# Optimization experiments

Hardware: AMD Instinct MI355X
Metric: run time of the kernel (lower is better)

## Reference

```python
import jax, jax.numpy as jnp
import numpy as np

NUM_HEADS = 16
D_MODEL = 1024


def setup_inputs() -> dict:
    key = jax.random.key(0)
    ks = jax.random.split(key, 12)
    B, S, D = 2, 2048, D_MODEL
    inp = {
        "query": jax.random.normal(ks[0], (B, S, D), dtype=jnp.float32),
        "key": jax.random.normal(ks[1], (B, S, D), dtype=jnp.float32),
        "value": jax.random.normal(ks[2], (B, S, D), dtype=jnp.float32),
        "mask": jax.random.randint(ks[3], (B, 1, S), 0, 2).astype(jnp.bool_),
    }
    # Linear layer params, stored as (in, out) so y = x @ W + b
    sd = 1.0 / np.sqrt(D)
    for i, nm in enumerate(["q", "k", "v", "o"]):
        inp[f"W{nm}"] = jax.random.uniform(ks[4 + 2 * i], (D, D), jnp.float32, -sd, sd)
        inp[f"b{nm}"] = jax.random.uniform(ks[5 + 2 * i], (D,), jnp.float32, -sd, sd)
    return inp


def _split_heads(x):
    # [B, S, D] -> [B, H, S, d_k]
    B, S, D = x.shape
    return x.reshape(B, S, NUM_HEADS, D // NUM_HEADS).transpose(0, 2, 1, 3)


def reference(query, key, value, mask, Wq, bq, Wk, bk, Wv, bv, Wo, bo):
    B, Sq, D = query.shape
    d_k = D // NUM_HEADS
    scale = 1.0 / np.sqrt(d_k)

    q = _split_heads(query @ Wq + bq)   # [B,H,Sq,dk]
    k = _split_heads(key @ Wk + bk)     # [B,H,Sk,dk]
    v = _split_heads(value @ Wv + bv)   # [B,H,Sk,dk]

    scores = jnp.einsum("bhqd,bhkd->bhqk", q, k) * scale  # [B,H,Sq,Sk]
    # mask: [B,1,Sk] bool, True = masked; broadcast over heads and queries
    scores = jnp.where(mask[:, None, :, :], -jnp.inf, scores)
    attn = jax.nn.softmax(scores, axis=-1)
    attn = jnp.nan_to_num(attn, nan=0.0)  # fully-masked rows -> 0 (matches torch)

    ctx = jnp.einsum("bhqk,bhkd->bhqd", attn, v)  # [B,H,Sq,dk]
    ctx = ctx.transpose(0, 2, 1, 3).reshape(B, Sq, D)  # combine heads
    out = ctx @ Wo + bo
    return out
```

## Files before the change

### kernel.cpp

```cpp
#include <hip/hip_runtime.h>


typedef unsigned short u16;
typedef __attribute__((ext_vector_type(8))) short bf16x8;
typedef __attribute__((ext_vector_type(4))) float f32x4;

static __device__ __forceinline__ u16 f2bf(float x) {
  union { float f; unsigned int i; } v; v.f = x;
  return (u16)((v.i + 0x8000u) >> 16);
}
static __device__ __forceinline__ float bf2f(u16 u) {
  union { unsigned int i; float f; } v; v.i = ((unsigned int)u) << 16; return v.f;
}

#define MFMA_B16(a, b, c) __builtin_amdgcn_mfma_f32_16x16x32_bf16((a), (b), (c), 0, 0, 0)

__global__ __launch_bounds__(256) void prep_w(
    const float* __restrict__ w0, const float* __restrict__ w1,
    const float* __restrict__ w2, const float* __restrict__ w3,
    u16* __restrict__ t0, u16* __restrict__ t1,
    u16* __restrict__ t2, u16* __restrict__ t3) {
  __shared__ u16 tile[64 * 68];
  const float* W; u16* T;
  switch (blockIdx.z) {
    case 0: W = w0; T = t0; break;
    case 1: W = w1; T = t1; break;
    case 2: W = w2; T = t2; break;
    default: W = w3; T = t3; break;
  }
  const int t = threadIdx.x;
  const int k0 = blockIdx.x * 64, n0 = blockIdx.y * 64;
#pragma unroll
  for (int it = 0; it < 4; ++it) {
    int idx = it * 256 + t;
    int r = idx >> 4, c4 = idx & 15;
    float4 v = *(const float4*)&W[(size_t)(k0 + r) * 1024 + n0 + c4 * 4];
    tile[r * 68 + c4 * 4 + 0] = f2bf(v.x);
    tile[r * 68 + c4 * 4 + 1] = f2bf(v.y);
    tile[r * 68 + c4 * 4 + 2] = f2bf(v.z);
    tile[r * 68 + c4 * 4 + 3] = f2bf(v.w);
  }
  __syncthreads();
#pragma unroll
  for (int it = 0; it < 2; ++it) {
    int idx = it * 256 + t;
    int n = idx >> 3, kc = idx & 7;
    bf16x8 pk;
#pragma unroll
    for (int j = 0; j < 8; ++j) pk[j] = (short)tile[(kc * 8 + j) * 68 + n];
    *(bf16x8*)&T[(size_t)(n0 + n) * 1024 + k0 + kc * 8] = pk;
  }
}

template <int MT, int AMODE, int OMODE>
__global__ __launch_bounds__(256) void gemm_bias(
    const void* a0v, const void* a1v, const void* a2v,
    const u16* __restrict__ Wt,
    const float* b0, const float* b1, const float* b2,
    void* o0, void* o1, void* o2) {
  __shared__ __align__(16) u16 As[MT * 32 * 32];
  __shared__ __align__(16) u16 Bs[128 * 32];
  const int t = threadIdx.x, wave = t >> 6, lane = t & 63;
  const int l15 = lane & 15, quad = lane >> 4;
  const int m0 = blockIdx.x * (MT * 32);
  const int n0 = blockIdx.y * 128;
  const int rg = (OMODE == 3) ? (n0 >> 10) : 0;
  const void* Av = (rg == 0) ? a0v : (rg == 1 ? a1v : a2v);
  const float* bp = (rg == 0) ? b0 : (rg == 1 ? b1 : b2);
  const int nb = (OMODE == 3) ? (n0 & 1023) : n0;
  const int wr = (wave >> 1) * (MT * 16), wc = (wave & 1) * 64;

  const f32x4 fz = {0.f, 0.f, 0.f, 0.f};
  f32x4 acc[MT][4];
#pragma unroll
  for (int mt = 0; mt < MT; ++mt)
#pragma unroll
    for (int nt = 0; nt < 4; ++nt) acc[mt][nt] = fz;

  float4 pa[MT / 2][2]; bf16x8 pab[MT / 2]; bf16x8 pb[2];
#pragma unroll
  for (int s = 0; s < MT / 2; ++s) {
    int idx = s * 256 + t, row = idx >> 2, seg = idx & 3;
    if (AMODE == 1) {
      const float* ap = (const float*)Av + (size_t)(m0 + row) * 1024 + seg * 8;
      pa[s][0] = *(const float4*)ap; pa[s][1] = *(const float4*)(ap + 4);
    } else {
      pab[s] = *(const bf16x8*)((const u16*)Av + (size_t)(m0 + row) * 1024 + seg * 8);
    }
  }
#pragma unroll
  for (int s = 0; s < 2; ++s) {
    int idx = s * 256 + t, row = idx >> 2, seg = idx & 3;
    pb[s] = *(const bf16x8*)&Wt[(size_t)(n0 + row) * 1024 + seg * 8];
  }

  for (int kb = 0; kb < 1024; kb += 32) {
    __syncthreads();
#pragma unroll
    for (int s = 0; s < MT / 2; ++s) {
      int idx = s * 256 + t, row = idx >> 2, seg = idx & 3;
      bf16x8 pk;
      if (AMODE == 1) {
        pk[0] = (short)f2bf(pa[s][0].x); pk[1] = (short)f2bf(pa[s][0].y);
        pk[2] = (short)f2bf(pa[s][0].z); pk[3] = (short)f2bf(pa[s][0].w);
        pk[4] = (short)f2bf(pa[s][1].x); pk[5] = (short)f2bf(pa[s][1].y);
        pk[6] = (short)f2bf(pa[s][1].z); pk[7] = (short)f2bf(pa[s][1].w);
      } else pk = pab[s];
      *(bf16x8*)&As[row * 32 + seg * 8] = pk;
    }
#pragma unroll
    for (int s = 0; s < 2; ++s) {
      int idx = s * 256 + t, row = idx >> 2, seg = idx & 3;
      *(bf16x8*)&Bs[row * 32 + seg * 8] = pb[s];
    }
    __syncthreads();
    const int kn = (kb + 32) & 1023;
#pragma unroll
    for (int s = 0; s < MT / 2; ++s) {
      int idx = s * 256 + t, row = idx >> 2, seg = idx & 3;
      if (AMODE == 1) {
        const float* ap = (const float*)Av + (size_t)(m0 + row) * 1024 + kn + seg * 8;
        pa[s][0] = *(const float4*)ap; pa[s][1] = *(const float4*)(ap + 4);
      } else {
        pab[s] = *(const bf16x8*)((const u16*)Av + (size_t)(m0 + row) * 1024 + kn + seg * 8);
      }
    }
#pragma unroll
    for (int s = 0; s < 2; ++s) {
      int idx = s * 256 + t, row = idx >> 2, seg = idx & 3;
      pb[s] = *(const bf16x8*)&Wt[(size_t)(n0 + row) * 1024 + kn + seg * 8];
    }
    bf16x8 a[MT], bfr[4];
#pragma unroll
    for (int mt = 0; mt < MT; ++mt)
      a[mt] = *(const bf16x8*)&As[(wr + mt * 16 + l15) * 32 + quad * 8];
#pragma unroll
    for (int nt = 0; nt < 4; ++nt)
      bfr[nt] = *(const bf16x8*)&Bs[(wc + nt * 16 + l15) * 32 + quad * 8];
#pragma unroll
    for (int mt = 0; mt < MT; ++mt)
#pragma unroll
      for (int nt = 0; nt < 4; ++nt)
        acc[mt][nt] = MFMA_B16(a[mt], bfr[nt], acc[mt][nt]);
  }

#pragma unroll
  for (int nt = 0; nt < 4; ++nt) {
    const int n = nb + wc + nt * 16 + l15;
    const float bv = bp[n];
#pragma unroll
    for (int mt = 0; mt < MT; ++mt)
#pragma unroll
      for (int r = 0; r < 4; ++r) {
        const int m = m0 + wr + mt * 16 + quad * 4 + r;
        const float val = acc[mt][nt][r] + bv;
        if (OMODE == 2) {
          ((float*)o0)[(size_t)m * 1024 + n] = val;
        } else if (OMODE == 0) {
          ((u16*)o0)[(size_t)m * 1024 + n] = f2bf(val);
        } else {
          if (rg == 0)      ((u16*)o0)[(size_t)m * 1024 + n] = f2bf(val);
          else if (rg == 1) ((u16*)o1)[(size_t)m * 1024 + n] = f2bf(val);
          else {
            const int h = n >> 6, d = n & 63, bb = m >> 11, ss = m & 2047;
            ((u16*)o2)[((size_t)(bb * 16 + h) * 64 + d) * 2048 + ss] = f2bf(val);
          }
        }
      }
  }
}

__global__ __launch_bounds__(512) void attn_fused(
    const u16* Q, const u16* __restrict__ K,
    const u16* __restrict__ Vt, const int* __restrict__ mask,
    u16* ctx) {
  __shared__ __align__(16) u16 Ks[128 * 72];
  __shared__ __align__(16) u16 Vs[64 * 136];
  __shared__ __align__(16) u16 Pl[8][16 * 136];
  __shared__ u16 Mb[2048];
  const int t = threadIdx.x, wave = t >> 6, lane = t & 63;
  const int l15 = lane & 15, quad = lane >> 4;
  const int bh = blockIdx.y, b = bh >> 4, h = bh & 15;
  const int q0 = blockIdx.x * 128 + wave * 16;
  const float cs = 0.125f * 1.44269504f;

#pragma unroll
  for (int i = 0; i < 4; ++i) {
    int idx = i * 512 + t;
    Mb[idx] = mask[b * 2048 + idx] ? 0xFF80 : 0;
  }

  const u16* Qp = Q + (size_t)(b * 2048 + q0) * 1024 + h * 64;
  const bf16x8 qf0 = *(const bf16x8*)(Qp + (size_t)l15 * 1024 + quad * 8);
  const bf16x8 qf1 = *(const bf16x8*)(Qp + (size_t)l15 * 1024 + 32 + quad * 8);

  const u16* Kbase = K + (size_t)(b * 2048) * 1024 + h * 64;
  const u16* Vbase = Vt + (size_t)bh * 64 * 2048;

  const int kr0 = t >> 3,        kc0 = (t & 7) * 8;
  const int kr1 = (512 + t) >> 3;
  const int vr0 = t >> 4,        vc0 = (t & 15) * 8;
  const int vr1 = (512 + t) >> 4;

  bf16x8 gk0 = *(const bf16x8*)&Kbase[(size_t)kr0 * 1024 + kc0];
  bf16x8 gk1 = *(const bf16x8*)&Kbase[(size_t)kr1 * 1024 + kc0];
  bf16x8 gv0 = *(const bf16x8*)&Vbase[(size_t)vr0 * 2048 + vc0];
  bf16x8 gv1 = *(const bf16x8*)&Vbase[(size_t)vr1 * 2048 + vc0];

  const f32x4 fz = {0.f, 0.f, 0.f, 0.f};
  f32x4 o[4];
  f32x4 lpart = fz;
#pragma unroll
  for (int i = 0; i < 4; ++i) o[i] = fz;

  for (int kt = 0; kt < 2048; kt += 128) {
    __syncthreads();
    *(bf16x8*)&Ks[kr0 * 72 + kc0] = gk0;
    *(bf16x8*)&Ks[kr1 * 72 + kc0] = gk1;
    *(bf16x8*)&Vs[vr0 * 136 + vc0] = gv0;
    *(bf16x8*)&Vs[vr1 * 136 + vc0] = gv1;
    __syncthreads();
    const int kn = (kt + 128) & 2047;
    gk0 = *(const bf16x8*)&Kbase[(size_t)(kn + kr0) * 1024 + kc0];
    gk1 = *(const bf16x8*)&Kbase[(size_t)(kn + kr1) * 1024 + kc0];
    gv0 = *(const bf16x8*)&Vbase[(size_t)vr0 * 2048 + kn + vc0];
    gv1 = *(const bf16x8*)&Vbase[(size_t)vr1 * 2048 + kn + vc0];

    float pv[8][4];
#pragma unroll
    for (int nt = 0; nt < 8; ++nt) {
      const int krow = nt * 16 + l15;
      bf16x8 k0 = *(const bf16x8*)&Ks[krow * 72 + quad * 8];
      bf16x8 k1 = *(const bf16x8*)&Ks[krow * 72 + 32 + quad * 8];
      f32x4 acc = MFMA_B16(qf0, k0, fz);
      acc = MFMA_B16(qf1, k1, acc);
      const float bias = bf2f(Mb[kt + krow]);
#pragma unroll
      for (int r = 0; r < 4; ++r) {
        float p = exp2f(fmaf(acc[r], cs, bias));
        pv[nt][r] = p; lpart[r] += p;
      }
    }
#pragma unroll
    for (int nt = 0; nt < 8; ++nt)
#pragma unroll
      for (int r = 0; r < 4; ++r)
        Pl[wave][(quad * 4 + r) * 136 + nt * 16 + l15] = f2bf(pv[nt][r]);
#pragma unroll
    for (int kc = 0; kc < 4; ++kc) {
      const bf16x8 pf = *(const bf16x8*)&Pl[wave][l15 * 136 + kc * 32 + quad * 8];
#pragma unroll
      for (int nt = 0; nt < 4; ++nt) {
        const bf16x8 vf = *(const bf16x8*)&Vs[(nt * 16 + l15) * 136 + kc * 32 + quad * 8];
        o[nt] = MFMA_B16(pf, vf, o[nt]);
      }
    }
  }
  float lrow[4];
#pragma unroll
  for (int r = 0; r < 4; ++r) {
    float sl = lpart[r];
    sl += __shfl_xor(sl, 1);
    sl += __shfl_xor(sl, 2);
    sl += __shfl_xor(sl, 4);
    sl += __shfl_xor(sl, 8);
    lrow[r] = sl;
  }
  u16* cp = ctx + (size_t)(b * 2048 + q0) * 1024 + h * 64;
#pragma unroll
  for (int r = 0; r < 4; ++r) {
    const bool ok = lrow[r] > 0.f;
    const float inv = ok ? 1.f / lrow[r] : 0.f;
#pragma unroll
    for (int nt = 0; nt < 4; ++nt)
      cp[(quad * 4 + r) * 1024 + nt * 16 + l15] = f2bf(ok ? o[nt][r] * inv : 0.f);
  }
}

extern "C" void kernel_launch(void* const* d_in, const int* in_sizes, int n_in,
                              void* d_out, int out_size, void* d_ws, size_t ws_size,
                              hipStream_t stream) {
  const float* q    = (const float*)d_in[0];
  const float* k    = (const float*)d_in[1];
  const float* v    = (const float*)d_in[2];
  const int*   mask = (const int*)d_in[3];
  const float* Wq = (const float*)d_in[4];  const float* bq = (const float*)d_in[5];
  const float* Wk = (const float*)d_in[6];  const float* bk = (const float*)d_in[7];
  const float* Wv = (const float*)d_in[8];  const float* bv = (const float*)d_in[9];
  const float* Wo = (const float*)d_in[10]; const float* bo = (const float*)d_in[11];

  char* ws = (char*)d_ws;
  u16*   Kp  = (u16*)(ws + ((size_t)0 << 20));
  u16*   Vt  = (u16*)(ws + ((size_t)8 << 20));
  float* O32 = (float*)ws;

  char* od = (char*)d_out;
  u16* ctx = (u16*)od;
  u16* WqT = (u16*)(od + ((size_t)8 << 20));
  u16* WkT = (u16*)(od + ((size_t)10 << 20));
  u16* WvT = (u16*)(od + ((size_t)12 << 20));
  u16* WoT = (u16*)(od + ((size_t)14 << 20));

  dim3 blk(256);
  prep_w<<<dim3(16, 16, 4), blk, 0, stream>>>(Wq, Wk, Wv, Wo, WqT, WkT, WvT, WoT);
  gemm_bias<4, 1, 3><<<dim3(32, 24), blk, 0, stream>>>(
      q, k, v, WqT, bq, bk, bv, (void*)ctx, (void*)Kp, (void*)Vt);
  attn_fused<<<dim3(16, 32), dim3(512), 0, stream>>>(ctx, Kp, Vt, mask, ctx);
  gemm_bias<2, 0, 2><<<dim3(64, 8), blk, 0, stream>>>(
      ctx, nullptr, nullptr, WoT, bo, nullptr, nullptr, (void*)O32, nullptr, nullptr);
  hipMemcpyAsync(d_out, O32, (size_t)out_size * sizeof(float),
                 hipMemcpyDeviceToDevice, stream);
}
```

Baseline: 267.8 us.

## Fold key mask into V projection and compute row sums with MFMA

The mask is applied by zeroing masked rows of V in the projection epilogue, so attention no longer adds a bias before exp. Row sums come from an extra MFMA against a 0/1 mask vector rather than per-lane adds and shuffles. Each wave now handles 32 query rows with 256-thread blocks, so every K/V fragment load from LDS is reused across two query tiles. S is computed transposed (K as the A operand), which lets P be stored in packed 64-bit writes. The costs are more registers per wave, fewer waves per block, and extra MFMA work for the row sums.

```diff
diff --git a/kernel.cpp b/kernel.cpp
--- a/kernel.cpp
+++ b/kernel.cpp
@@ -8,9 +8,6 @@
 static __device__ __forceinline__ u16 f2bf(float x) {
   union { float f; unsigned int i; } v; v.f = x;
   return (u16)((v.i + 0x8000u) >> 16);
-}
-static __device__ __forceinline__ float bf2f(u16 u) {
-  union { unsigned int i; float f; } v; v.i = ((unsigned int)u) << 16; return v.f;
 }
 
 #define MFMA_B16(a, b, c) __builtin_amdgcn_mfma_f32_16x16x32_bf16((a), (b), (c), 0, 0, 0)
@@ -57,7 +54,7 @@
     const void* a0v, const void* a1v, const void* a2v,
     const u16* __restrict__ Wt,
     const float* b0, const float* b1, const float* b2,
-    void* o0, void* o1, void* o2) {
+    void* o0, void* o1, void* o2, const int* msk) {
   __shared__ __align__(16) u16 As[MT * 32 * 32];
   __shared__ __align__(16) u16 Bs[128 * 32];
   const int t = threadIdx.x, wave = t >> 6, lane = t & 63;
@@ -153,7 +150,7 @@
 #pragma unroll
       for (int r = 0; r < 4; ++r) {
         const int m = m0 + wr + mt * 16 + quad * 4 + r;
-        const float val = acc[mt][nt][r] + bv;
+        float val = acc[mt][nt][r] + bv;
         if (OMODE == 2) {
           ((float*)o0)[(size_t)m * 1024 + n] = val;
         } else if (OMODE == 0) {
@@ -163,6 +160,7 @@
           else if (rg == 1) ((u16*)o1)[(size_t)m * 1024 + n] = f2bf(val);
           else {
             const int h = n >> 6, d = n & 63, bb = m >> 11, ss = m & 2047;
+            if (msk[bb * 2048 + ss]) val = 0.f;
             ((u16*)o2)[((size_t)(bb * 16 + h) * 64 + d) * 2048 + ss] = f2bf(val);
           }
         }
@@ -170,110 +168,116 @@
   }
 }
 
-__global__ __launch_bounds__(512) void attn_fused(
+__global__ __launch_bounds__(256) void attn_fused(
     const u16* Q, const u16* __restrict__ K,
     const u16* __restrict__ Vt, const int* __restrict__ mask,
     u16* ctx) {
   __shared__ __align__(16) u16 Ks[128 * 72];
   __shared__ __align__(16) u16 Vs[64 * 136];
-  __shared__ __align__(16) u16 Pl[8][16 * 136];
-  __shared__ u16 Mb[2048];
+  __shared__ __align__(16) u16 Pl[4][32 * 136];
+  __shared__ __align__(16) u16 Ml[2048];
   const int t = threadIdx.x, wave = t >> 6, lane = t & 63;
   const int l15 = lane & 15, quad = lane >> 4;
   const int bh = blockIdx.y, b = bh >> 4, h = bh & 15;
-  const int q0 = blockIdx.x * 128 + wave * 16;
+  const int q0 = blockIdx.x * 128 + wave * 32;
   const float cs = 0.125f * 1.44269504f;
 
 #pragma unroll
-  for (int i = 0; i < 4; ++i) {
-    int idx = i * 512 + t;
-    Mb[idx] = mask[b * 2048 + idx] ? 0xFF80 : 0;
+  for (int i = 0; i < 8; ++i) {
+    int idx = i * 256 + t;
+    Ml[idx] = mask[b * 2048 + idx] ? 0 : 0x3F80;
   }
 
   const u16* Qp = Q + (size_t)(b * 2048 + q0) * 1024 + h * 64;
-  const bf16x8 qf0 = *(const bf16x8*)(Qp + (size_t)l15 * 1024 + quad * 8);
-  const bf16x8 qf1 = *(const bf16x8*)(Qp + (size_t)l15 * 1024 + 32 + quad * 8);
+  bf16x8 qf[2][2];
+#pragma unroll
+  for (int qh = 0; qh < 2; ++qh) {
+    qf[qh][0] = *(const bf16x8*)(Qp + (size_t)(qh * 16 + l15) * 1024 + quad * 8);
+    qf[qh][1] = *(const bf16x8*)(Qp + (size_t)(qh * 16 + l15) * 1024 + 32 + quad * 8);
+  }
 
   const u16* Kbase = K + (size_t)(b * 2048) * 1024 + h * 64;
   const u16* Vbase = Vt + (size_t)bh * 64 * 2048;
 
-  const int kr0 = t >> 3,        kc0 = (t & 7) * 8;
-  const int kr1 = (512 + t) >> 3;
-  const int vr0 = t >> 4,        vc0 = (t & 15) * 8;
-  const int vr1 = (512 + t) >> 4;
-
-  bf16x8 gk0 = *(const bf16x8*)&Kbase[(size_t)kr0 * 1024 + kc0];
-  bf16x8 gk1 = *(const bf16x8*)&Kbase[(size_t)kr1 * 1024 + kc0];
-  bf16x8 gv0 = *(const bf16x8*)&Vbase[(size_t)vr0 * 2048 + vc0];
-  bf16x8 gv1 = *(const bf16x8*)&Vbase[(size_t)vr1 * 2048 + vc0];
+  bf16x8 gk[4], gv[4];
+#pragma unroll
+  for (int s = 0; s < 4; ++s) {
+    int ki = s * 256 + t, kr = ki >> 3, kc = (ki & 7) * 8;
+    int vi = s * 256 + t, vr = vi >> 4, vc = (vi & 15) * 8;
+    gk[s] = *(const bf16x8*)&Kbase[(size_t)kr * 1024 + kc];
+    gv[s] = *(const bf16x8*)&Vbase[(size_t)vr * 2048 + vc];
+  }
 
   const f32x4 fz = {0.f, 0.f, 0.f, 0.f};
-  f32x4 o[4];
-  f32x4 lpart = fz;
-#pragma unroll
-  for (int i = 0; i < 4; ++i) o[i] = fz;
+  f32x4 o[2][4];
+  f32x4 lacc[2];
+#pragma unroll
+  for (int qh = 0; qh < 2; ++qh) {
+    lacc[qh] = fz;
+#pragma unroll
+    for (int nt = 0; nt < 4; ++nt) o[qh][nt] = fz;
+  }
 
   for (int kt = 0; kt < 2048; kt += 128) {
     __syncthreads();
-    *(bf16x8*)&Ks[kr0 * 72 + kc0] = gk0;
-    *(bf16x8*)&Ks[kr1 * 72 + kc0] = gk1;
-    *(bf16x8*)&Vs[vr0 * 136 + vc0] = gv0;
-    *(bf16x8*)&Vs[vr1 * 136 + vc0] = gv1;
+#pragma unroll
+    for (int s = 0; s < 4; ++s) {
+      int ki = s * 256 + t, kr = ki >> 3, kc = (ki & 7) * 8;
+      int vi = s * 256 + t, vr = vi >> 4, vc = (vi & 15) * 8;
+      *(bf16x8*)&Ks[kr * 72 + kc] = gk[s];
+      *(bf16x8*)&Vs[vr * 136 + vc] = gv[s];
+    }
     __syncthreads();
     const int kn = (kt + 128) & 2047;
-    gk0 = *(const bf16x8*)&Kbase[(size_t)(kn + kr0) * 1024 + kc0];
-    gk1 = *(const bf16x8*)&Kbase[(size_t)(kn + kr1) * 1024 + kc0];
-    gv0 = *(const bf16x8*)&Vbase[(size_t)vr0 * 2048 + kn + vc0];
-    gv1 = *(const bf16x8*)&Vbase[(size_t)vr1 * 2048 + kn + vc0];
-
-    float pv[8][4];
-#pragma unroll
-    for (int nt = 0; nt < 8; ++nt) {
-      const int krow = nt * 16 + l15;
-      bf16x8 k0 = *(const bf16x8*)&Ks[krow * 72 + quad * 8];
-      bf16x8 k1 = *(const bf16x8*)&Ks[krow * 72 + 32 + quad * 8];
-      f32x4 acc = MFMA_B16(qf0, k0, fz);
-      acc = MFMA_B16(qf1, k1, acc);
-      const float bias = bf2f(Mb[kt + krow]);
-#pragma unroll
-      for (int r = 0; r < 4; ++r) {
-        float p = exp2f(fmaf(acc[r], cs, bias));
-        pv[nt][r] = p; lpart[r] += p;
+#pragma unroll
+    for (int s = 0; s < 4; ++s) {
+      int ki = s * 256 + t, kr = ki >> 3, kc = (ki & 7) * 8;
+      int vi = s * 256 + t, vr = vi >> 4, vc = (vi & 15) * 8;
+      gk[s] = *(const bf16x8*)&Kbase[(size_t)(kn + kr) * 1024 + kc];
+      gv[s] = *(const bf16x8*)&Vbase[(size_t)vr * 2048 + kn + vc];
+    }
+
+#pragma unroll
+    for (int qh = 0; qh < 2; ++qh) {
+#pragma unroll
+      for (int kb8 = 0; kb8 < 8; ++kb8) {
+        const int krow = kb8 * 16 + l15;
+        bf16x8 kf0 = *(const bf16x8*)&Ks[krow * 72 + quad * 8];
+        bf16x8 kf1 = *(const bf16x8*)&Ks[krow * 72 + 32 + quad * 8];
+        f32x4 st = MFMA_B16(kf0, qf[qh][0], fz);
+        st = MFMA_B16(kf1, qf[qh][1], st);
+        union { u16 h[4]; unsigned long long u; } pk;
+#pragma unroll
+        for (int r = 0; r < 4; ++r) pk.h[r] = f2bf(exp2f(st[r] * cs));
+        *(unsigned long long*)&Pl[wave][(qh * 16 + l15) * 136 + kb8 * 16 + quad * 4] = pk.u;
       }
     }
 #pragma unroll
-    for (int nt = 0; nt < 8; ++nt)
-#pragma unroll
-      for (int r = 0; r < 4; ++r)
-        Pl[wave][(quad * 4 + r) * 136 + nt * 16 + l15] = f2bf(pv[nt][r]);
-#pragma unroll
     for (int kc = 0; kc < 4; ++kc) {
-      const bf16x8 pf = *(const bf16x8*)&Pl[wave][l15 * 136 + kc * 32 + quad * 8];
-#pragma unroll
-      for (int nt = 0; nt < 4; ++nt) {
-        const bf16x8 vf = *(const bf16x8*)&Vs[(nt * 16 + l15) * 136 + kc * 32 + quad * 8];
-        o[nt] = MFMA_B16(pf, vf, o[nt]);
+      const bf16x8 mlf = *(const bf16x8*)&Ml[kt + kc * 32 + quad * 8];
+#pragma unroll
+      for (int qh = 0; qh < 2; ++qh) {
+        const bf16x8 pf = *(const bf16x8*)&Pl[wave][(qh * 16 + l15) * 136 + kc * 32 + quad * 8];
+        lacc[qh] = MFMA_B16(pf, mlf, lacc[qh]);
+#pragma unroll
+        for (int nt = 0; nt < 4; ++nt) {
+          const bf16x8 vf = *(const bf16x8*)&Vs[(nt * 16 + l15) * 136 + kc * 32 + quad * 8];
+          o[qh][nt] = MFMA_B16(pf, vf, o[qh][nt]);
+        }
       }
     }
   }
-  float lrow[4];
-#pragma unroll
-  for (int r = 0; r < 4; ++r) {
-    float sl = lpart[r];
-    sl += __shfl_xor(sl, 1);
-    sl += __shfl_xor(sl, 2);
-    sl += __shfl_xor(sl, 4);
-    sl += __shfl_xor(sl, 8);
-    lrow[r] = sl;
-  }
-  u16* cp = ctx + (size_t)(b * 2048 + q0) * 1024 + h * 64;
-#pragma unroll
-  for (int r = 0; r < 4; ++r) {
-    const bool ok = lrow[r] > 0.f;
-    const float inv = ok ? 1.f / lrow[r] : 0.f;
-#pragma unroll
-    for (int nt = 0; nt < 4; ++nt)
-      cp[(quad * 4 + r) * 1024 + nt * 16 + l15] = f2bf(ok ? o[nt][r] * inv : 0.f);
+#pragma unroll
+  for (int qh = 0; qh < 2; ++qh) {
+    u16* cp = ctx + (size_t)(b * 2048 + q0 + qh * 16) * 1024 + h * 64;
+#pragma unroll
+    for (int r = 0; r < 4; ++r) {
+      const bool ok = lacc[qh][r] > 0.f;
+      const float inv = ok ? 1.f / lacc[qh][r] : 0.f;
+#pragma unroll
+      for (int nt = 0; nt < 4; ++nt)
+        cp[(quad * 4 + r) * 1024 + nt * 16 + l15] = f2bf(ok ? o[qh][nt][r] * inv : 0.f);
+    }
   }
 }
 
@@ -304,10 +308,10 @@
   dim3 blk(256);
   prep_w<<<dim3(16, 16, 4), blk, 0, stream>>>(Wq, Wk, Wv, Wo, WqT, WkT, WvT, WoT);
   gemm_bias<4, 1, 3><<<dim3(32, 24), blk, 0, stream>>>(
-      q, k, v, WqT, bq, bk, bv, (void*)ctx, (void*)Kp, (void*)Vt);
-  attn_fused<<<dim3(16, 32), dim3(512), 0, stream>>>(ctx, Kp, Vt, mask, ctx);
+      q, k, v, WqT, bq, bk, bv, (void*)ctx, (void*)Kp, (void*)Vt, mask);
+  attn_fused<<<dim3(16, 32), blk, 0, stream>>>(ctx, Kp, Vt, mask, ctx);
   gemm_bias<2, 0, 2><<<dim3(64, 8), blk, 0, stream>>>(
-      ctx, nullptr, nullptr, WoT, bo, nullptr, nullptr, (void*)O32, nullptr, nullptr);
+      ctx, nullptr, nullptr, WoT, bo, nullptr, nullptr, (void*)O32, nullptr, nullptr, mask);
   hipMemcpyAsync(d_out, O32, (size_t)out_size * sizeof(float),
                  hipMemcpyDeviceToDevice, stream);
 }
```

Result: slower. 281.7 us (+5.2%).
